# Optimization experiments

Hardware: AMD Instinct MI355X
Metric: run time of the kernel (lower is better)

The kernel has to match this reference:

```python
import jax, jax.numpy as jnp
import numpy as np

HIDDEN = 1024
QKV = 1024
HEADS = 16
HEAD_DIM = QKV // HEADS
B, S = 4, 4096


def setup_inputs() -> dict:
    key = jax.random.key(0)
    ks = jax.random.split(key, 8)
    s = 1.0 / np.sqrt(HIDDEN)
    return {
        "x": jax.random.normal(ks[0], (B, S, HIDDEN), dtype=jnp.float32),
        "mask": jnp.ones((B, S, 1), dtype=jnp.float32),
        "Wq": jax.random.uniform(ks[1], (HIDDEN, QKV), jnp.float32, -s, s),
        "bq": jax.random.uniform(ks[2], (QKV,), jnp.float32, -s, s),
        "Wk": jax.random.uniform(ks[3], (HIDDEN, QKV), jnp.float32, -s, s),
        "bk": jax.random.uniform(ks[4], (QKV,), jnp.float32, -s, s),
        "Wv": jax.random.uniform(ks[5], (HIDDEN, QKV), jnp.float32, -s, s),
        "bv": jax.random.uniform(ks[6], (QKV,), jnp.float32, -s, s),
    }


def _split_heads(t):
    # [B, S, QKV] -> [B, H, S, D]
    b, s, _ = t.shape
    return t.reshape(b, s, HEADS, HEAD_DIM).transpose(0, 2, 1, 3)


def reference(x, mask, Wq, bq, Wk, bk, Wv, bv):
    q = (x @ Wq + bq) * mask  # [B, S, QKV]
    k = (x @ Wk + bk) * mask
    v = (x @ Wv + bv) * mask
    q, k, v = _split_heads(q), _split_heads(k), _split_heads(v)  # [B,H,S,D]
    # k^T @ v : [B, H, D, D]
    kv = jnp.einsum('bhsd,bhse->bhde', k, v)
    # per-batch norm constant from mask sum
    norm = mask.sum(axis=(-1, -2))  # [B]
    norm = 1.0 / jnp.sqrt(norm * HEAD_DIM)
    kv = kv * norm[:, None, None, None]
    # dropout is identity in eval mode
    out = jnp.einsum('bhsd,bhde->bhse', q, kv)  # [B, H, S, D]
    out = out.transpose(0, 2, 1, 3).reshape(B, S, QKV)
    return out
```

## Files before the change

### kernel.cpp

```cpp
#include <hip/hip_runtime.h>
#include <stdint.h>

#define HIDDEN 1024
#define SEQ 4096
#define BATCH 4
#define HEADS 16
#define HDIM 64
#define M_TOT (BATCH * SEQ)
#define NCH 4
#define NT64 16

typedef __bf16 bf16x8 __attribute__((ext_vector_type(8)));
typedef float f32x4 __attribute__((ext_vector_type(4)));
typedef unsigned short u16x8 __attribute__((ext_vector_type(8)));

static __device__ __forceinline__ unsigned short f2bf(float f) {
  union { float f; uint32_t u; } v; v.f = f;
  uint32_t u = v.u;
  uint32_t r = (u + 0x7fffu + ((u >> 16) & 1u)) >> 16;
  return (unsigned short)r;
}
static __device__ __forceinline__ void load_lds16(const void* g, void* l) {
  __builtin_amdgcn_global_load_lds(
      (__attribute__((address_space(1))) void*)(g),
      (__attribute__((address_space(3))) void*)(l), 16, 0, 0);
}

__global__ __launch_bounds__(256) void prep_k(
    const float* __restrict__ x, unsigned short* __restrict__ xb,
    const float* __restrict__ Wk, const float* __restrict__ Wv,
    const float* __restrict__ Wq,
    unsigned short* __restrict__ Bt, unsigned short* __restrict__ Wqt,
    const float* __restrict__ bk, const float* __restrict__ bv,
    float* __restrict__ bkv,
    const float* __restrict__ mask, float* __restrict__ norm) {
  const int bid = blockIdx.x;
  const int tid = threadIdx.x;
  __shared__ float ts[64][65];
  if (bid < 8192) {
    int idx = bid * 256 + tid;
    const float4* xv = (const float4*)x;
    float4 a = xv[(size_t)idx * 2];
    float4 b = xv[(size_t)idx * 2 + 1];
    u16x8 o;
    o[0] = f2bf(a.x); o[1] = f2bf(a.y); o[2] = f2bf(a.z); o[3] = f2bf(a.w);
    o[4] = f2bf(b.x); o[5] = f2bf(b.y); o[6] = f2bf(b.z); o[7] = f2bf(b.w);
    *(u16x8*)(xb + (size_t)idx * 8) = o;
  } else if (bid < 8960) {
    int idx = bid - 8192;
    int z = idx >> 8, rem = idx & 255;
    const float* W = (z == 0) ? Wk : (z == 1) ? Wv : Wq;
    unsigned short* out = (z == 2) ? Wqt : (Bt + (size_t)z * HIDDEN * HIDDEN);
    int n0 = (rem & 15) * 64, k0 = (rem >> 4) * 64;
    int c = tid & 63, rq = tid >> 6;
    for (int i = 0; i < 16; ++i) {
      int r = i * 4 + rq;
      ts[r][c] = W[(size_t)(k0 + r) * HIDDEN + n0 + c];
    }
    __syncthreads();
    for (int i = 0; i < 16; ++i) {
      int n = i * 4 + rq;
      out[(size_t)(n0 + n) * HIDDEN + k0 + c] = f2bf(ts[c][n]);
    }
  } else if (bid < 8968) {
    int i = (bid - 8960) * 256 + tid;
    bkv[i] = (i < HIDDEN) ? bk[i] : bv[i - HIDDEN];
  } else {
    int b = bid - 8968;
    float s = 0.f;
    for (int i = tid; i < SEQ; i += 256) s += mask[b * SEQ + i];
    for (int off = 32; off; off >>= 1) s += __shfl_down(s, off);
    __shared__ float wsum[4];
    if ((tid & 63) == 0) wsum[tid >> 6] = s;
    __syncthreads();
    if (tid == 0) {
      float t = wsum[0] + wsum[1] + wsum[2] + wsum[3];
      norm[b] = rsqrtf(t * (float)HDIM);
    }
  }
}

template <int OUT_MODE>
__global__ __launch_bounds__(512, 2) void gemm256_k(
    const unsigned short* __restrict__ A, const unsigned short* __restrict__ Bt,
    const float* __restrict__ bias, const float* __restrict__ mask,
    const unsigned short* __restrict__ kvt,
    void* __restrict__ C, int nbn) {
  __shared__ unsigned short smem[65536];

  const int nwg = gridDim.x;
  const int bid = blockIdx.x;
  const int wg = (bid & 7) * (nwg >> 3) + (bid >> 3);
  const int row0 = (wg / nbn) * 256;
  const int col0 = (wg % nbn) * 256;

  const int tid = threadIdx.x;
  const int wave = tid >> 6;
  const int lane = tid & 63;
  const int wm = wave >> 2;
  const int wn = wave & 3;
  const int lr = lane & 15;
  const int hi = lane >> 4;

  const int srow = tid >> 3;
  const int scol = ((tid & 7) ^ (srow & 7)) * 8;
  const unsigned short* sA = A + (size_t)(row0 + srow) * HIDDEN + scol;
  const unsigned short* sB = Bt + (size_t)(col0 + srow) * HIDDEN + scol;
  const int ldst = tid * 8;

#define STAGE(half, tt, isB) { \
    int dst_ = ((tt)&1) * 32768 + (isB) * 16384 + (half) * 8192 + ldst; \
    const unsigned short* src_ = ((isB) ? sB : sA) + (size_t)(half) * 128 * HIDDEN + (tt) * 64; \
    load_lds16(src_, &smem[dst_]); \
    load_lds16(src_ + (size_t)64 * HIDDEN, &smem[dst_ + 4096]); }

  const int chunk0 = (hi ^ (lr & 7)) * 8;
  const int chunk1 = ((4 + hi) ^ (lr & 7)) * 8;
  const int arow = (wm * 128 + lr) * 64;
  const int brow = 16384 + (wn * 64 + lr) * 64;

  f32x4 acc[8][4];
#pragma unroll
  for (int i = 0; i < 8; ++i)
#pragma unroll
    for (int j = 0; j < 4; ++j) acc[i][j] = (f32x4){0.f, 0.f, 0.f, 0.f};

  STAGE(0, 0, 0) STAGE(1, 0, 0) STAGE(0, 0, 1) STAGE(1, 0, 1)
  STAGE(0, 1, 1) STAGE(1, 1, 1)
  asm volatile("s_waitcnt vmcnt(4)" ::: "memory");
  __builtin_amdgcn_s_barrier();

  bf16x8 af[4][2], b0f[2][2], b1f[2][2];
  for (int t = 0; t < NT64; ++t) {
    const int bb = (t & 1) * 32768;
#pragma unroll
    for (int rf = 0; rf < 4; ++rf) {
      af[rf][0] = *(const bf16x8*)&smem[bb + arow + rf * 1024 + chunk0];
      af[rf][1] = *(const bf16x8*)&smem[bb + arow + rf * 1024 + chunk1];
    }
#pragma unroll
    for (int cf = 0; cf < 2; ++cf) {
      b0f[cf][0] = *(const bf16x8*)&smem[bb + brow + cf * 1024 + chunk0];
      b0f[cf][1] = *(const bf16x8*)&smem[bb + brow + cf * 1024 + chunk1];
    }
    if (t + 1 < NT64) STAGE(0, t + 1, 0)
    __builtin_amdgcn_s_setprio(1);
#pragma unroll
    for (int rf = 0; rf < 4; ++rf)
#pragma unroll
      for (int cf = 0; cf < 2; ++cf)
#pragma unroll
        for (int kh = 0; kh < 2; ++kh)
          acc[rf][cf] = __builtin_amdgcn_mfma_f32_16x16x32_bf16(af[rf][kh], b0f[cf][kh], acc[rf][cf], 0, 0, 0);
    __builtin_amdgcn_s_setprio(0);
    asm volatile("" ::: "memory");
    __builtin_amdgcn_s_barrier();
#pragma unroll
    for (int cf = 0; cf < 2; ++cf) {
      b1f[cf][0] = *(const bf16x8*)&smem[bb + brow + 2048 + cf * 1024 + chunk0];
      b1f[cf][1] = *(const bf16x8*)&smem[bb + brow + 2048 + cf * 1024 + chunk1];
    }
    if (t + 1 < NT64) STAGE(1, t + 1, 0)
    __builtin_amdgcn_s_setprio(1);
#pragma unroll
    for (int rf = 0; rf < 4; ++rf)
#pragma unroll
      for (int cf = 0; cf < 2; ++cf)
#pragma unroll
        for (int kh = 0; kh < 2; ++kh)
          acc[rf][2 + cf] = __builtin_amdgcn_mfma_f32_16x16x32_bf16(af[rf][kh], b1f[cf][kh], acc[rf][2 + cf], 0, 0, 0);
    __builtin_amdgcn_s_setprio(0);
    asm volatile("" ::: "memory");
    __builtin_amdgcn_s_barrier();
#pragma unroll
    for (int rf = 0; rf < 4; ++rf) {
      af[rf][0] = *(const bf16x8*)&smem[bb + arow + 4096 + rf * 1024 + chunk0];
      af[rf][1] = *(const bf16x8*)&smem[bb + arow + 4096 + rf * 1024 + chunk1];
    }
    __builtin_amdgcn_s_setprio(1);
#pragma unroll
    for (int rf = 0; rf < 4; ++rf)
#pragma unroll
      for (int cf = 0; cf < 2; ++cf)
#pragma unroll
        for (int kh = 0; kh < 2; ++kh)
          acc[4 + rf][cf] = __builtin_amdgcn_mfma_f32_16x16x32_bf16(af[rf][kh], b0f[cf][kh], acc[4 + rf][cf], 0, 0, 0);
    __builtin_amdgcn_s_setprio(0);
    asm volatile("" ::: "memory");
    __builtin_amdgcn_s_barrier();
    if (t + 2 < NT64) { STAGE(0, t + 2, 1) STAGE(1, t + 2, 1) }
    __builtin_amdgcn_s_setprio(1);
#pragma unroll
    for (int rf = 0; rf < 4; ++rf)
#pragma unroll
      for (int cf = 0; cf < 2; ++cf)
#pragma unroll
        for (int kh = 0; kh < 2; ++kh)
          acc[4 + rf][2 + cf] = __builtin_amdgcn_mfma_f32_16x16x32_bf16(af[rf][kh], b1f[cf][kh], acc[4 + rf][2 + cf], 0, 0, 0);
    __builtin_amdgcn_s_setprio(0);
    if (t < NT64 - 3) asm volatile("s_waitcnt vmcnt(4)" ::: "memory");
    else              asm volatile("s_waitcnt vmcnt(0)" ::: "memory");
    __builtin_amdgcn_s_barrier();
  }

  float bcol[4];
#pragma unroll
  for (int an = 0; an < 4; ++an)
    bcol[an] = bias[col0 + wn * 64 + (an >> 1) * 32 + (an & 1) * 16 + lr];

  if (OUT_MODE == 2) {
    const int b = row0 >> 12;
    const int s0 = (row0 & 4095) + wm * 128;
    unsigned short* wt = &smem[wave * 4096];
    unsigned short* KVt = (unsigned short*)C;
#pragma unroll
    for (int half = 0; half < 2; ++half) {
#pragma unroll
      for (int am4 = 0; am4 < 4; ++am4) {
#pragma unroll
        for (int j = 0; j < 4; ++j) {
          int r = am4 * 16 + hi * 4 + j;
          float mrow = mask[row0 + wm * 128 + half * 64 + r];
#pragma unroll
          for (int an = 0; an < 4; ++an) {
            int c = (an >> 1) * 32 + (an & 1) * 16 + lr;
            wt[c * 64 + (r ^ ((c & 7) << 3))] =
                f2bf((acc[half * 4 + am4][an][j] + bcol[an]) * mrow);
          }
        }
      }
      asm volatile("s_waitcnt lgkmcnt(0)" ::: "memory");
#pragma unroll
      for (int i = 0; i < 8; ++i) {
        int flat = i * 64 + lane;
        int c = flat >> 3, rq = flat & 7;
        uint4 vv = *(const uint4*)&wt[c * 64 + ((rq * 8) ^ ((c & 7) << 3))];
        *(uint4*)&KVt[((size_t)(col0 + wn * 64 + c) * 4 + b) * 4096 + s0 + half * 64 + rq * 8] = vv;
      }
      asm volatile("s_waitcnt lgkmcnt(0)" ::: "memory");
    }
  } else {
    float* Og = (float*)C;
    const int b = row0 >> 12;
    const int bh = b * 16 + (col0 >> 6) + wn;
    unsigned short* wt = &smem[wave * 4096];
    bf16x8 kvf[4][2];
#pragma unroll
    for (int et = 0; et < 4; ++et) {
      kvf[et][0] = *(const bf16x8*)&kvt[(size_t)bh * 4096 + (et * 16 + lr) * 64 + hi * 8];
      kvf[et][1] = *(const bf16x8*)&kvt[(size_t)bh * 4096 + (et * 16 + lr) * 64 + 32 + hi * 8];
    }
#pragma unroll
    for (int half = 0; half < 2; ++half) {
#pragma unroll
      for (int am4 = 0; am4 < 4; ++am4) {
#pragma unroll
        for (int j = 0; j < 4; ++j) {
          int r = am4 * 16 + hi * 4 + j;
          float mrow = mask[row0 + wm * 128 + half * 64 + r];
#pragma unroll
          for (int an = 0; an < 4; ++an) {
            int c = (an >> 1) * 32 + (an & 1) * 16 + lr;
            wt[r * 64 + (c ^ ((r & 7) << 3))] =
                f2bf((acc[half * 4 + am4][an][j] + bcol[an]) * mrow);
          }
        }
      }
      asm volatile("s_waitcnt lgkmcnt(0)" ::: "memory");
      f32x4 oacc[4][4];
#pragma unroll
      for (int g = 0; g < 4; ++g) {
        bf16x8 a0 = *(const bf16x8*)&wt[(g * 16 + lr) * 64 + chunk0];
        bf16x8 a1 = *(const bf16x8*)&wt[(g * 16 + lr) * 64 + chunk1];
#pragma unroll
        for (int et = 0; et < 4; ++et) {
          oacc[g][et] = (f32x4){0.f, 0.f, 0.f, 0.f};
          oacc[g][et] = __builtin_amdgcn_mfma_f32_16x16x32_bf16(a0, kvf[et][0], oacc[g][et], 0, 0, 0);
          oacc[g][et] = __builtin_amdgcn_mfma_f32_16x16x32_bf16(a1, kvf[et][1], oacc[g][et], 0, 0, 0);
        }
      }
#pragma unroll
      for (int g = 0; g < 4; ++g)
#pragma unroll
        for (int et = 0; et < 4; ++et)
#pragma unroll
          for (int j = 0; j < 4; ++j)
            __builtin_nontemporal_store(oacc[g][et][j],
                &Og[(size_t)(row0 + wm * 128 + half * 64 + g * 16 + hi * 4 + j) * 1024
                    + col0 + wn * 64 + et * 16 + lr]);
      asm volatile("s_waitcnt lgkmcnt(0)" ::: "memory");
    }
  }
#undef STAGE
}

__global__ __launch_bounds__(256) void kvpart2_k(const unsigned short* __restrict__ KVt,
                                                 float* __restrict__ part) {
  const int bh = blockIdx.x, ch = blockIdx.y;
  const int b = bh >> 4, h = bh & 15;
  __shared__ unsigned short tl[32768];
  const int tid = threadIdx.x;
  const int wave = tid >> 6, lane = tid & 63;
  const int lr = lane & 15, hi = lane >> 4;

  const int r0 = tid >> 3;
  const int cc0 = ((tid & 7) ^ (r0 & 7)) * 8;
  const int r1 = 32 + r0;
  const int cc1 = ((tid & 7) ^ (r1 & 7)) * 8;
  const unsigned short* A0 = KVt + ((size_t)(h * 64 + r0) * 4 + b) * 4096 + ch * 1024 + cc0;
  const unsigned short* A1 = KVt + ((size_t)(h * 64 + r1) * 4 + b) * 4096 + ch * 1024 + cc1;
  const unsigned short* B0 = KVt + ((size_t)(1024 + h * 64 + r0) * 4 + b) * 4096 + ch * 1024 + cc0;
  const unsigned short* B1 = KVt + ((size_t)(1024 + h * 64 + r1) * 4 + b) * 4096 + ch * 1024 + cc1;

#define KSTAGE(tt) { int bb2 = ((tt) & 3) * 8192; \
    load_lds16(A0 + (tt) * 64, &tl[bb2 + tid * 8]); \
    load_lds16(A1 + (tt) * 64, &tl[bb2 + 2048 + tid * 8]); \
    load_lds16(B0 + (tt) * 64, &tl[bb2 + 4096 + tid * 8]); \
    load_lds16(B1 + (tt) * 64, &tl[bb2 + 6144 + tid * 8]); }

  const int ra = wave * 16 + lr;
  const int aoff = ra * 64;
  const int ach0 = (hi ^ (ra & 7)) * 8, ach1 = ((4 + hi) ^ (ra & 7)) * 8;

  f32x4 acc4[4];
#pragma unroll
  for (int nt = 0; nt < 4; ++nt) acc4[nt] = (f32x4){0.f, 0.f, 0.f, 0.f};

  KSTAGE(0) KSTAGE(1)
  asm volatile("s_waitcnt vmcnt(4)" ::: "memory");
  __builtin_amdgcn_s_barrier();
  for (int t = 0; t < 16; ++t) {
    const int bb = (t & 3) * 8192;
    if (t + 2 < 16) KSTAGE(t + 2)
    bf16x8 a0 = *(const bf16x8*)&tl[bb + aoff + ach0];
    bf16x8 a1 = *(const bf16x8*)&tl[bb + aoff + ach1];
    bf16x8 bf0[4], bf1[4];
#pragma unroll
    for (int nt = 0; nt < 4; ++nt) {
      int rb = nt * 16 + lr;
      bf0[nt] = *(const bf16x8*)&tl[bb + 4096 + rb * 64 + ((hi ^ (rb & 7)) * 8)];
      bf1[nt] = *(const bf16x8*)&tl[bb + 4096 + rb * 64 + (((4 + hi) ^ (rb & 7)) * 8)];
    }
#pragma unroll
    for (int nt = 0; nt < 4; ++nt) {
      acc4[nt] = __builtin_amdgcn_mfma_f32_16x16x32_bf16(a0, bf0[nt], acc4[nt], 0, 0, 0);
      acc4[nt] = __builtin_amdgcn_mfma_f32_16x16x32_bf16(a1, bf1[nt], acc4[nt], 0, 0, 0);
    }
    if (t < 14) asm volatile("s_waitcnt vmcnt(4)" ::: "memory");
    else        asm volatile("s_waitcnt vmcnt(0)" ::: "memory");
    __builtin_amdgcn_s_barrier();
  }
  float* dst = part + ((size_t)(ch * 64 + bh)) * 4096;
#pragma unroll
  for (int nt = 0; nt < 4; ++nt)
#pragma unroll
    for (int j = 0; j < 4; ++j)
      dst[(wave * 16 + hi * 4 + j) * 64 + nt * 16 + lr] = acc4[nt][j];
#undef KSTAGE
}

__global__ void kvreduce_k(const float* __restrict__ part, const float* __restrict__ norm,
                           unsigned short* __restrict__ kvt) {
  int idx4 = (blockIdx.x * 256 + threadIdx.x) * 4;
  int bh = idx4 >> 12, rem = idx4 & 4095;
  int e = rem >> 6, d0 = rem & 63;
  float s0 = 0.f, s1 = 0.f, s2 = 0.f, s3 = 0.f;
#pragma unroll
  for (int ch = 0; ch < NCH; ++ch) {
    const float* p = part + ((size_t)(ch * 64 + bh)) * 4096 + e;
    s0 += p[(d0 + 0) * 64];
    s1 += p[(d0 + 1) * 64];
    s2 += p[(d0 + 2) * 64];
    s3 += p[(d0 + 3) * 64];
  }
  float nb = norm[bh >> 4];
  ushort4 o;
  o.x = f2bf(s0 * nb); o.y = f2bf(s1 * nb); o.z = f2bf(s2 * nb); o.w = f2bf(s3 * nb);
  *(ushort4*)&kvt[idx4] = o;
}

extern "C" void kernel_launch(void* const* d_in, const int* in_sizes, int n_in,
                              void* d_out, int out_size, void* d_ws, size_t ws_size,
                              hipStream_t stream) {
  const float* x = (const float*)d_in[0];
  const float* mask = (const float*)d_in[1];
  const float* Wq = (const float*)d_in[2];
  const float* bq = (const float*)d_in[3];
  const float* Wk = (const float*)d_in[4];
  const float* bk = (const float*)d_in[5];
  const float* Wv = (const float*)d_in[6];
  const float* bv = (const float*)d_in[7];
  float* out = (float*)d_out;

  char* w = (char*)d_ws;
  unsigned short* xb = (unsigned short*)w;   w += (size_t)M_TOT * HIDDEN * 2;
  unsigned short* Bt = (unsigned short*)w;   w += (size_t)2048 * HIDDEN * 2;
  unsigned short* Wqt = (unsigned short*)w;  w += (size_t)HIDDEN * HIDDEN * 2;
  unsigned short* KVt = (unsigned short*)w;  w += (size_t)2048 * BATCH * SEQ * 2;
  float* part = (float*)w;                   w += (size_t)NCH * 64 * 4096 * 4;
  unsigned short* kvt = (unsigned short*)w;  w += (size_t)64 * 4096 * 2;
  float* bkv = (float*)w;                    w += 2048 * 4;
  float* norm = (float*)w;                   w += 64;

  prep_k<<<dim3(8972), dim3(256), 0, stream>>>(x, xb, Wk, Wv, Wq, Bt, Wqt, bk, bv, bkv, mask, norm);
  gemm256_k<2><<<dim3(512), dim3(512), 0, stream>>>(xb, Bt, bkv, mask, nullptr, (void*)KVt, 8);
  kvpart2_k<<<dim3(64, NCH), dim3(256), 0, stream>>>(KVt, part);
  kvreduce_k<<<dim3(256), dim3(256), 0, stream>>>(part, norm, kvt);
  gemm256_k<4><<<dim3(256), dim3(512), 0, stream>>>(xb, Wqt, bq, mask, kvt, (void*)out, 4);
}
```

Before: 154.4 us.

## Shrink GEMM tiles to 256x128 with K=32 steps and higher occupancy

Reworks the projection GEMM kernel from a 256x256 tile with K=64 double-buffered stages and an interleaved four-phase schedule to a 256x128 tile with K=32 stages, a simpler single-phase loop and half the LDS. Launch bounds rise to 4 blocks per CU and the grids double. The aim is more concurrent workgroups and better latency hiding through occupancy rather than a hand-scheduled pipeline. In exchange, each K step now ends with a full vmcnt(0) wait plus a barrier, there are twice as many iterations, and the smaller tile means less operand reuse and more global traffic.

```diff
diff --git a/kernel.cpp b/kernel.cpp
--- a/kernel.cpp
+++ b/kernel.cpp
@@ -8,7 +8,7 @@
 #define HDIM 64
 #define M_TOT (BATCH * SEQ)
 #define NCH 4
-#define NT64 16
+#define NT 32
 
 typedef __bf16 bf16x8 __attribute__((ext_vector_type(8)));
 typedef float f32x4 __attribute__((ext_vector_type(4)));
@@ -81,169 +81,110 @@
 }
 
 template <int OUT_MODE>
-__global__ __launch_bounds__(512, 2) void gemm256_k(
+__global__ __launch_bounds__(512, 4) void gemm256_k(
     const unsigned short* __restrict__ A, const unsigned short* __restrict__ Bt,
     const float* __restrict__ bias, const float* __restrict__ mask,
     const unsigned short* __restrict__ kvt,
     void* __restrict__ C, int nbn) {
-  __shared__ unsigned short smem[65536];
+  __shared__ unsigned short smem[32768];
 
   const int nwg = gridDim.x;
   const int bid = blockIdx.x;
   const int wg = (bid & 7) * (nwg >> 3) + (bid >> 3);
   const int row0 = (wg / nbn) * 256;
-  const int col0 = (wg % nbn) * 256;
+  const int col0 = (wg % nbn) * 128;
 
   const int tid = threadIdx.x;
   const int wave = tid >> 6;
   const int lane = tid & 63;
-  const int wm = wave >> 2;
-  const int wn = wave & 3;
+  const int wm = wave >> 1;
+  const int wn = wave & 1;
   const int lr = lane & 15;
   const int hi = lane >> 4;
 
-  const int srow = tid >> 3;
-  const int scol = ((tid & 7) ^ (srow & 7)) * 8;
-  const unsigned short* sA = A + (size_t)(row0 + srow) * HIDDEN + scol;
-  const unsigned short* sB = Bt + (size_t)(col0 + srow) * HIDDEN + scol;
-  const int ldst = tid * 8;
-
-#define STAGE(half, tt, isB) { \
-    int dst_ = ((tt)&1) * 32768 + (isB) * 16384 + (half) * 8192 + ldst; \
-    const unsigned short* src_ = ((isB) ? sB : sA) + (size_t)(half) * 128 * HIDDEN + (tt) * 64; \
-    load_lds16(src_, &smem[dst_]); \
-    load_lds16(src_ + (size_t)64 * HIDDEN, &smem[dst_ + 4096]); }
-
-  const int chunk0 = (hi ^ (lr & 7)) * 8;
-  const int chunk1 = ((4 + hi) ^ (lr & 7)) * 8;
-  const int arow = (wm * 128 + lr) * 64;
-  const int brow = 16384 + (wn * 64 + lr) * 64;
-
-  f32x4 acc[8][4];
-#pragma unroll
-  for (int i = 0; i < 8; ++i)
+  const int srow = tid >> 2;
+  const int sc = ((tid & 3) ^ ((srow >> 1) & 3)) * 8;
+  const unsigned short* sA0 = A + (size_t)(row0 + srow) * HIDDEN + sc;
+  const unsigned short* sA1 = A + (size_t)(row0 + 128 + srow) * HIDDEN + sc;
+  const unsigned short* sB0 = Bt + (size_t)(col0 + srow) * HIDDEN + sc;
+
+#define STAGE_A(tt) { int dst_ = ((tt) & 1) * 12288 + tid * 8; \
+    load_lds16(sA0 + (size_t)(tt) * 32, &smem[dst_]); \
+    load_lds16(sA1 + (size_t)(tt) * 32, &smem[dst_ + 4096]); }
+#define STAGE_B(tt) { int dst_ = ((tt) & 1) * 12288 + 8192 + tid * 8; \
+    load_lds16(sB0 + (size_t)(tt) * 32, &smem[dst_]); }
+
+  const int kch = (hi ^ ((lr >> 1) & 3)) * 8;
+  const int aoff = (wm * 64 + lr) * 32;
+  const int boff = 8192 + (wn * 64 + lr) * 32;
+
+  f32x4 acc[4][4];
+#pragma unroll
+  for (int i = 0; i < 4; ++i)
 #pragma unroll
     for (int j = 0; j < 4; ++j) acc[i][j] = (f32x4){0.f, 0.f, 0.f, 0.f};
 
-  STAGE(0, 0, 0) STAGE(1, 0, 0) STAGE(0, 0, 1) STAGE(1, 0, 1)
-  STAGE(0, 1, 1) STAGE(1, 1, 1)
-  asm volatile("s_waitcnt vmcnt(4)" ::: "memory");
+  STAGE_A(0) STAGE_B(0)
+  asm volatile("s_waitcnt vmcnt(0)" ::: "memory");
   __builtin_amdgcn_s_barrier();
 
-  bf16x8 af[4][2], b0f[2][2], b1f[2][2];
-  for (int t = 0; t < NT64; ++t) {
-    const int bb = (t & 1) * 32768;
-#pragma unroll
-    for (int rf = 0; rf < 4; ++rf) {
-      af[rf][0] = *(const bf16x8*)&smem[bb + arow + rf * 1024 + chunk0];
-      af[rf][1] = *(const bf16x8*)&smem[bb + arow + rf * 1024 + chunk1];
-    }
-#pragma unroll
-    for (int cf = 0; cf < 2; ++cf) {
-      b0f[cf][0] = *(const bf16x8*)&smem[bb + brow + cf * 1024 + chunk0];
-      b0f[cf][1] = *(const bf16x8*)&smem[bb + brow + cf * 1024 + chunk1];
-    }
-    if (t + 1 < NT64) STAGE(0, t + 1, 0)
+  for (int t = 0; t < NT; ++t) {
+    const int bb = (t & 1) * 12288;
+    if (t + 1 < NT) { STAGE_A(t + 1) STAGE_B(t + 1) }
+    bf16x8 af[4], bf[4];
+#pragma unroll
+    for (int rf = 0; rf < 4; ++rf)
+      af[rf] = *(const bf16x8*)&smem[bb + aoff + rf * 512 + kch];
+#pragma unroll
+    for (int cf = 0; cf < 4; ++cf)
+      bf[cf] = *(const bf16x8*)&smem[bb + boff + cf * 512 + kch];
     __builtin_amdgcn_s_setprio(1);
 #pragma unroll
     for (int rf = 0; rf < 4; ++rf)
 #pragma unroll
-      for (int cf = 0; cf < 2; ++cf)
-#pragma unroll
-        for (int kh = 0; kh < 2; ++kh)
-          acc[rf][cf] = __builtin_amdgcn_mfma_f32_16x16x32_bf16(af[rf][kh], b0f[cf][kh], acc[rf][cf], 0, 0, 0);
+      for (int cf = 0; cf < 4; ++cf)
+        acc[rf][cf] = __builtin_amdgcn_mfma_f32_16x16x32_bf16(af[rf], bf[cf], acc[rf][cf], 0, 0, 0);
     __builtin_amdgcn_s_setprio(0);
-    asm volatile("" ::: "memory");
+    asm volatile("s_waitcnt vmcnt(0)" ::: "memory");
     __builtin_amdgcn_s_barrier();
-#pragma unroll
-    for (int cf = 0; cf < 2; ++cf) {
-      b1f[cf][0] = *(const bf16x8*)&smem[bb + brow + 2048 + cf * 1024 + chunk0];
-      b1f[cf][1] = *(const bf16x8*)&smem[bb + brow + 2048 + cf * 1024 + chunk1];
-    }
-    if (t + 1 < NT64) STAGE(1, t + 1, 0)
-    __builtin_amdgcn_s_setprio(1);
-#pragma unroll
-    for (int rf = 0; rf < 4; ++rf)
-#pragma unroll
-      for (int cf = 0; cf < 2; ++cf)
-#pragma unroll
-        for (int kh = 0; kh < 2; ++kh)
-          acc[rf][2 + cf] = __builtin_amdgcn_mfma_f32_16x16x32_bf16(af[rf][kh], b1f[cf][kh], acc[rf][2 + cf], 0, 0, 0);
-    __builtin_amdgcn_s_setprio(0);
-    asm volatile("" ::: "memory");
-    __builtin_amdgcn_s_barrier();
-#pragma unroll
-    for (int rf = 0; rf < 4; ++rf) {
-      af[rf][0] = *(const bf16x8*)&smem[bb + arow + 4096 + rf * 1024 + chunk0];
-      af[rf][1] = *(const bf16x8*)&smem[bb + arow + 4096 + rf * 1024 + chunk1];
-    }
-    __builtin_amdgcn_s_setprio(1);
-#pragma unroll
-    for (int rf = 0; rf < 4; ++rf)
-#pragma unroll
-      for (int cf = 0; cf < 2; ++cf)
-#pragma unroll
-        for (int kh = 0; kh < 2; ++kh)
-          acc[4 + rf][cf] = __builtin_amdgcn_mfma_f32_16x16x32_bf16(af[rf][kh], b0f[cf][kh], acc[4 + rf][cf], 0, 0, 0);
-    __builtin_amdgcn_s_setprio(0);
-    asm volatile("" ::: "memory");
-    __builtin_amdgcn_s_barrier();
-    if (t + 2 < NT64) { STAGE(0, t + 2, 1) STAGE(1, t + 2, 1) }
-    __builtin_amdgcn_s_setprio(1);
-#pragma unroll
-    for (int rf = 0; rf < 4; ++rf)
-#pragma unroll
-      for (int cf = 0; cf < 2; ++cf)
-#pragma unroll
-        for (int kh = 0; kh < 2; ++kh)
-          acc[4 + rf][2 + cf] = __builtin_amdgcn_mfma_f32_16x16x32_bf16(af[rf][kh], b1f[cf][kh], acc[4 + rf][2 + cf], 0, 0, 0);
-    __builtin_amdgcn_s_setprio(0);
-    if (t < NT64 - 3) asm volatile("s_waitcnt vmcnt(4)" ::: "memory");
-    else              asm volatile("s_waitcnt vmcnt(0)" ::: "memory");
-    __builtin_amdgcn_s_barrier();
   }
 
   float bcol[4];
 #pragma unroll
-  for (int an = 0; an < 4; ++an)
-    bcol[an] = bias[col0 + wn * 64 + (an >> 1) * 32 + (an & 1) * 16 + lr];
+  for (int cf = 0; cf < 4; ++cf)
+    bcol[cf] = bias[col0 + wn * 64 + cf * 16 + lr];
+
+  unsigned short* wt = &smem[wave * 4096];
 
   if (OUT_MODE == 2) {
     const int b = row0 >> 12;
-    const int s0 = (row0 & 4095) + wm * 128;
-    unsigned short* wt = &smem[wave * 4096];
+    const int s0 = (row0 & 4095) + wm * 64;
     unsigned short* KVt = (unsigned short*)C;
 #pragma unroll
-    for (int half = 0; half < 2; ++half) {
-#pragma unroll
-      for (int am4 = 0; am4 < 4; ++am4) {
-#pragma unroll
-        for (int j = 0; j < 4; ++j) {
-          int r = am4 * 16 + hi * 4 + j;
-          float mrow = mask[row0 + wm * 128 + half * 64 + r];
-#pragma unroll
-          for (int an = 0; an < 4; ++an) {
-            int c = (an >> 1) * 32 + (an & 1) * 16 + lr;
-            wt[c * 64 + (r ^ ((c & 7) << 3))] =
-                f2bf((acc[half * 4 + am4][an][j] + bcol[an]) * mrow);
-          }
+    for (int rf = 0; rf < 4; ++rf)
+#pragma unroll
+      for (int j = 0; j < 4; ++j) {
+        int r = rf * 16 + hi * 4 + j;
+        float mrow = mask[row0 + wm * 64 + r];
+#pragma unroll
+        for (int cf = 0; cf < 4; ++cf) {
+          int c = cf * 16 + lr;
+          wt[c * 64 + (r ^ ((c & 7) << 3))] = f2bf((acc[rf][cf][j] + bcol[cf]) * mrow);
         }
       }
-      asm volatile("s_waitcnt lgkmcnt(0)" ::: "memory");
-#pragma unroll
-      for (int i = 0; i < 8; ++i) {
-        int flat = i * 64 + lane;
-        int c = flat >> 3, rq = flat & 7;
-        uint4 vv = *(const uint4*)&wt[c * 64 + ((rq * 8) ^ ((c & 7) << 3))];
-        *(uint4*)&KVt[((size_t)(col0 + wn * 64 + c) * 4 + b) * 4096 + s0 + half * 64 + rq * 8] = vv;
-      }
-      asm volatile("s_waitcnt lgkmcnt(0)" ::: "memory");
-    }
+    asm volatile("s_waitcnt lgkmcnt(0)" ::: "memory");
+#pragma unroll
+    for (int i = 0; i < 8; ++i) {
+      int flat = i * 64 + lane;
+      int c = flat >> 3, rq = flat & 7;
+      uint4 vv = *(const uint4*)&wt[c * 64 + ((rq * 8) ^ ((c & 7) << 3))];
+      *(uint4*)&KVt[((size_t)(col0 + wn * 64 + c) * 4 + b) * 4096 + s0 + rq * 8] = vv;
+    }
+    asm volatile("s_waitcnt lgkmcnt(0)" ::: "memory");
   } else {
     float* Og = (float*)C;
     const int b = row0 >> 12;
     const int bh = b * 16 + (col0 >> 6) + wn;
-    unsigned short* wt = &smem[wave * 4096];
     bf16x8 kvf[4][2];
 #pragma unroll
     for (int et = 0; et < 4; ++et) {
@@ -251,47 +192,40 @@
       kvf[et][1] = *(const bf16x8*)&kvt[(size_t)bh * 4096 + (et * 16 + lr) * 64 + 32 + hi * 8];
     }
 #pragma unroll
-    for (int half = 0; half < 2; ++half) {
-#pragma unroll
-      for (int am4 = 0; am4 < 4; ++am4) {
-#pragma unroll
-        for (int j = 0; j < 4; ++j) {
-          int r = am4 * 16 + hi * 4 + j;
-          float mrow = mask[row0 + wm * 128 + half * 64 + r];
-#pragma unroll
-          for (int an = 0; an < 4; ++an) {
-            int c = (an >> 1) * 32 + (an & 1) * 16 + lr;
-            wt[r * 64 + (c ^ ((r & 7) << 3))] =
-                f2bf((acc[half * 4 + am4][an][j] + bcol[an]) * mrow);
-          }
+    for (int rf = 0; rf < 4; ++rf)
+#pragma unroll
+      for (int j = 0; j < 4; ++j) {
+        int r = rf * 16 + hi * 4 + j;
+        float mrow = mask[row0 + wm * 64 + r];
+#pragma unroll
+        for (int cf = 0; cf < 4; ++cf) {
+          int c = cf * 16 + lr;
+          wt[r * 64 + (c ^ ((r & 7) << 3))] = f2bf((acc[rf][cf][j] + bcol[cf]) * mrow);
         }
       }
-      asm volatile("s_waitcnt lgkmcnt(0)" ::: "memory");
-      f32x4 oacc[4][4];
-#pragma unroll
-      for (int g = 0; g < 4; ++g) {
-        bf16x8 a0 = *(const bf16x8*)&wt[(g * 16 + lr) * 64 + chunk0];
-        bf16x8 a1 = *(const bf16x8*)&wt[(g * 16 + lr) * 64 + chunk1];
-#pragma unroll
-        for (int et = 0; et < 4; ++et) {
-          oacc[g][et] = (f32x4){0.f, 0.f, 0.f, 0.f};
-          oacc[g][et] = __builtin_amdgcn_mfma_f32_16x16x32_bf16(a0, kvf[et][0], oacc[g][et], 0, 0, 0);
-          oacc[g][et] = __builtin_amdgcn_mfma_f32_16x16x32_bf16(a1, kvf[et][1], oacc[g][et], 0, 0, 0);
-        }
+    asm volatile("s_waitcnt lgkmcnt(0)" ::: "memory");
+    const int echunk0 = (hi ^ (lr & 7)) * 8;
+    const int echunk1 = ((4 + hi) ^ (lr & 7)) * 8;
+#pragma unroll
+    for (int g = 0; g < 4; ++g) {
+      bf16x8 a0 = *(const bf16x8*)&wt[(g * 16 + lr) * 64 + echunk0];
+      bf16x8 a1 = *(const bf16x8*)&wt[(g * 16 + lr) * 64 + echunk1];
+#pragma unroll
+      for (int et = 0; et < 4; ++et) {
+        f32x4 o4 = (f32x4){0.f, 0.f, 0.f, 0.f};
+        o4 = __builtin_amdgcn_mfma_f32_16x16x32_bf16(a0, kvf[et][0], o4, 0, 0, 0);
+        o4 = __builtin_amdgcn_mfma_f32_16x16x32_bf16(a1, kvf[et][1], o4, 0, 0, 0);
+#pragma unroll
+        for (int j = 0; j < 4; ++j)
+          __builtin_nontemporal_store(o4[j],
+              &Og[(size_t)(row0 + wm * 64 + g * 16 + hi * 4 + j) * 1024
+                  + col0 + wn * 64 + et * 16 + lr]);
       }
-#pragma unroll
-      for (int g = 0; g < 4; ++g)
-#pragma unroll
-        for (int et = 0; et < 4; ++et)
-#pragma unroll
-          for (int j = 0; j < 4; ++j)
-            __builtin_nontemporal_store(oacc[g][et][j],
-                &Og[(size_t)(row0 + wm * 128 + half * 64 + g * 16 + hi * 4 + j) * 1024
-                    + col0 + wn * 64 + et * 16 + lr]);
-      asm volatile("s_waitcnt lgkmcnt(0)" ::: "memory");
-    }
-  }
-#undef STAGE
+    }
+    asm volatile("s_waitcnt lgkmcnt(0)" ::: "memory");
+  }
+#undef STAGE_A
+#undef STAGE_B
 }
 
 __global__ __launch_bounds__(256) void kvpart2_k(const unsigned short* __restrict__ KVt,
@@ -403,8 +337,8 @@
   float* norm = (float*)w;                   w += 64;
 
   prep_k<<<dim3(8972), dim3(256), 0, stream>>>(x, xb, Wk, Wv, Wq, Bt, Wqt, bk, bv, bkv, mask, norm);
-  gemm256_k<2><<<dim3(512), dim3(512), 0, stream>>>(xb, Bt, bkv, mask, nullptr, (void*)KVt, 8);
+  gemm256_k<2><<<dim3(1024), dim3(512), 0, stream>>>(xb, Bt, bkv, mask, nullptr, (void*)KVt, 16);
   kvpart2_k<<<dim3(64, NCH), dim3(256), 0, stream>>>(KVt, part);
   kvreduce_k<<<dim3(256), dim3(256), 0, stream>>>(part, norm, kvt);
-  gemm256_k<4><<<dim3(256), dim3(512), 0, stream>>>(xb, Wqt, bq, mask, kvt, (void*)out, 4);
-}
+  gemm256_k<4><<<dim3(512), dim3(512), 0, stream>>>(xb, Wqt, bq, mask, kvt, (void*)out, 8);
+}
```

New measurement: 168.8 us. 1.09x slower.
